# Kernel optimization log

Hardware: AMD Instinct MI355X
Metric: run time of the kernel (lower is better)

The kernel has to match this reference:

```python
import jax, jax.numpy as jnp
import numpy as np

EPS = 1e-5
STW = 10   # short_term_window_size
L = 12     # mlp_layers


def gru_step(h, x, Wi, Wh, bi, bh):
    # torch nn.GRU cell, gate order (r, z, n)
    gi = x @ Wi.T + bi            # [B, 3H]
    gh = h @ Wh.T + bh            # [B, 3H]
    ir, iz, inn = jnp.split(gi, 3, axis=-1)
    hr, hz, hn = jnp.split(gh, 3, axis=-1)
    r = jax.nn.sigmoid(ir + hr)
    z = jax.nn.sigmoid(iz + hz)
    n = jnp.tanh(inn + r * hn)
    return (1.0 - z) * n + z * h


def mlp_mini(m, seq_W, seq_b, ln_a, ln_b, out_W, out_b, mrg_W, mrg_b):
    # m: [B, S, H] -> siMLPe_mini -> [B, 1, C]
    f = jnp.swapaxes(m, 1, 2)                 # [B, H, S]
    for l in range(L):                        # TransMLP: temporal FC + spatial LN + residual
        y = f @ seq_W[l].T + seq_b[l]         # Linear over seq axis S
        mu = y.mean(axis=1, keepdims=True)    # LN over feature ('spatial') axis H
        var = ((y - mu) ** 2).mean(axis=1, keepdims=True)
        y = (y - mu) / jnp.sqrt(var + EPS) * ln_a[l][None, :, None] + ln_b[l][None, :, None]
        f = f + y
    f = jnp.swapaxes(f, 1, 2) @ out_W.T + out_b   # [B, S, C]  motion_fc_out
    f = jnp.swapaxes(f, 1, 2) @ mrg_W.T + mrg_b   # [B, C, 1]  temporal_merge_fc
    return jnp.swapaxes(f, 1, 2)                  # [B, 1, C]


def _forward(x, gru_Wi, gru_Wh, gru_bi, gru_bh, enc_W, enc_b,
             seq_W, seq_b, ln_alpha, ln_beta, out_W, out_b, merge_W, merge_b):
    B, T, C = x.shape
    H = gru_Wh.shape[1]

    @jax.checkpoint
    def enc_step(h, xt):
        return gru_step(h, xt, gru_Wi, gru_Wh, gru_bi, gru_bh), None

    h0 = jnp.zeros((B, H), dtype=x.dtype)
    h_enc, _ = jax.lax.scan(enc_step, h0, jnp.swapaxes(x[:, :-1, :], 0, 1))

    last_frame = x[:, -1, :]
    # encode_history=True: one GRU step on the last frame; resulting state discarded
    window_history = gru_step(h_enc, last_frame, gru_Wi, gru_Wh, gru_bi, gru_bh)[:, None, :]  # [B,1,H]

    buf0 = x[:, -STW:, :]  # sliding short-term window buffer [B, STW, C]

    @jax.checkpoint
    def dec_step(carry, _):
        h, last, buf = carry
        h = gru_step(h, last, gru_Wi, gru_Wh, gru_bi, gru_bh)
        dec = h[:, None, :]                        # [B, 1, H]
        wst = buf @ enc_W.T + enc_b                # fc_encoder: [B, STW, H]
        mlp_in = jnp.concatenate([window_history, wst, dec], axis=1)  # [B, STW+2, H]
        new = mlp_mini(mlp_in, seq_W, seq_b, ln_alpha, ln_beta, out_W, out_b, mrg_W=merge_W, mrg_b=merge_b)
        new = new + last[:, None, :]               # recursive_residual=True
        newf = new[:, 0, :]
        buf = jnp.concatenate([buf[:, 1:, :], new], axis=1)
        return (h, newf, buf), newf

    _, outs = jax.lax.scan(dec_step, (h_enc, last_frame, buf0), None, length=T)
    return jnp.swapaxes(outs, 0, 1)  # [B, T, C]


def setup_inputs() -> dict:
    key = jax.random.key(0)
    B, T, C, H = 1024, 64, 66, 1024
    S = STW + 2
    ks = jax.random.split(key, 16)

    def g(k, shape, scale):
        return jax.random.normal(k, shape, dtype=jnp.float32) * scale

    return {
        "x": g(ks[0], (B, T, C), 1.0),
        "gru_Wi": g(ks[1], (3 * H, C), 0.05),
        "gru_Wh": g(ks[2], (3 * H, H), 0.02),
        "gru_bi": jnp.zeros((3 * H,), jnp.float32),
        "gru_bh": jnp.zeros((3 * H,), jnp.float32),
        "enc_W": g(ks[3], (H, C), 0.05),
        "enc_b": jnp.zeros((H,), jnp.float32),
        "seq_W": g(ks[4], (L, S, S), 0.2),
        "seq_b": jnp.zeros((L, S), jnp.float32),
        "ln_alpha": jnp.ones((L, H), jnp.float32),
        "ln_beta": jnp.zeros((L, H), jnp.float32),
        "out_W": g(ks[5], (C, H), 0.02),
        "out_b": jnp.zeros((C,), jnp.float32),
        "merge_W": g(ks[6], (1, S), 0.2),
        "merge_b": jnp.zeros((1,), jnp.float32),
    }


def reference(x, gru_Wi, gru_Wh, gru_bi, gru_bh, enc_W, enc_b,
              seq_W, seq_b, ln_alpha, ln_beta, out_W, out_b, merge_W, merge_b):
    return _forward(x, gru_Wi, gru_Wh, gru_bi, gru_bh, enc_W, enc_b,
                    seq_W, seq_b, ln_alpha, ln_beta, out_W, out_b, merge_W, merge_b)
```

## Files before the change

### kernel.cpp

```cpp
#include <hip/hip_runtime.h>
#include <hip/hip_bf16.h>
#include <cstddef>
#include <cstdint>

#define BB 1024
#define TT 64
#define CC 66
#define HH 1024
#define SS 12
#define LL 12
#define XROW (TT*CC)
#define KSEG 16

typedef __attribute__((ext_vector_type(8))) __bf16 bfrag;
typedef __attribute__((ext_vector_type(4))) float f32x4;
typedef __attribute__((ext_vector_type(8))) short s8v;
typedef __attribute__((ext_vector_type(2))) float f2;

__device__ __forceinline__ unsigned short f2bf(float f) {
  unsigned int u = __builtin_bit_cast(unsigned int, f);
  unsigned int r = u + 0x7FFFu + ((u >> 16) & 1u);
  return (unsigned short)(r >> 16);
}
__device__ __forceinline__ float bf2f(unsigned short h) {
  unsigned int u = ((unsigned int)h) << 16;
  return __builtin_bit_cast(float, u);
}

__device__ __forceinline__ void gload16(const void* g, void* l) {
  __builtin_amdgcn_global_load_lds(
      (const __attribute__((address_space(1))) unsigned int*)g,
      (__attribute__((address_space(3))) unsigned int*)l, 16, 0, 0);
}

template<int CTRL, int RM>
__device__ __forceinline__ float dppadd(float v) {
  int x = __builtin_amdgcn_update_dpp(0, __builtin_bit_cast(int, v),
                                      CTRL, RM, 0xF, true);
  return v + __builtin_bit_cast(float, x);
}
__device__ __forceinline__ float wave_sum63(float v) {
  v = dppadd<0x111, 0xF>(v);
  v = dppadd<0x112, 0xF>(v);
  v = dppadd<0x114, 0xF>(v);
  v = dppadd<0x118, 0xF>(v);
  v = dppadd<0x142, 0xa>(v);
  v = dppadd<0x143, 0xc>(v);
  return v;
}

__global__ __launch_bounds__(256) void gru_mfma(
    const unsigned short* __restrict__ Ahi, const unsigned short* __restrict__ Alo,
    const float* __restrict__ hprev,
    const unsigned short* __restrict__ Xhi, const unsigned short* __restrict__ Xlo,
    const unsigned short* __restrict__ Whi, const unsigned short* __restrict__ Wlo,
    const float* __restrict__ bi, const float* __restrict__ bh,
    float* __restrict__ hout_f32,
    unsigned short* __restrict__ hout_hi, unsigned short* __restrict__ hout_lo)
{
  __shared__ __align__(16) unsigned short AsH[3][64*32];
  __shared__ __align__(16) unsigned short AsL[3][64*32];
  __shared__ __align__(16) unsigned short BsH[3][128*32];
  __shared__ __align__(16) unsigned short BsL[3][128*32];

  const int tid = threadIdx.x, lane = tid & 63, wid = tid >> 6;
  const int bid = blockIdx.x;
  const int idx = bid >> 3;
  const int jb = (bid & 7) * 4 + (idx & 3);
  const int b0 = (idx >> 2) * 64;
  const int wm = wid >> 1, wn = wid & 1;
  const int aR = lane >> 2, aC = lane & 3;

  auto stage = [&](int bs, int kc) {
    const unsigned short *shi, *slo; size_t go;
    int row = wid * 16 + aR;
    if (kc < 32) {
      go = (size_t)(b0 + row) * 1024 + (size_t)kc * 32 + aC * 8;
      shi = Ahi; slo = Alo;
    } else {
      go = (size_t)(b0 + row) * 96 + (size_t)(kc - 32) * 32 + aC * 8;
      shi = Xhi; slo = Xlo;
    }
    gload16(shi + go, &AsH[bs][wid * 512]);
    gload16(slo + go, &AsL[bs][wid * 512]);
    size_t base = ((size_t)jb * 35 + kc) * 4096;
    size_t go0 = base + (size_t)(wid * 32 + aR) * 32 + aC * 8;
    gload16(Whi + go0,       &BsH[bs][wid * 1024]);
    gload16(Whi + go0 + 512, &BsH[bs][wid * 1024 + 512]);
    gload16(Wlo + go0,       &BsL[bs][wid * 1024]);
    gload16(Wlo + go0 + 512, &BsL[bs][wid * 1024 + 512]);
  };

  int offA[2], offB[4];
  #pragma unroll
  for (int mh = 0; mh < 2; ++mh) {
    int r = wm * 32 + mh * 16 + (lane & 15);
    int cb = (lane >> 4) ^ (r & 3);
    offA[mh] = r * 32 + cb * 8;
  }
  #pragma unroll
  for (int g = 0; g < 4; ++g) {
    int r = wn * 64 + g * 16 + (lane & 15);
    int cb = (lane >> 4) ^ (r & 3);
    offB[g] = r * 32 + cb * 8;
  }

  f32x4 acc[2][4] = {};

  stage(0, 0);
  stage(1, 1);

  int cur = 0;
  for (int kc = 0; kc < 34; ++kc) {
    asm volatile("s_waitcnt vmcnt(6)" ::: "memory");
    __builtin_amdgcn_s_barrier();
    asm volatile("" ::: "memory");

    bfrag ah[2], al[2], bhf[4], blf[4];
    #pragma unroll
    for (int mh = 0; mh < 2; ++mh) {
      ah[mh] = __builtin_bit_cast(bfrag, *(const s8v*)(&AsH[cur][offA[mh]]));
      al[mh] = __builtin_bit_cast(bfrag, *(const s8v*)(&AsL[cur][offA[mh]]));
    }
    #pragma unroll
    for (int g = 0; g < 4; ++g) {
      bhf[g] = __builtin_bit_cast(bfrag, *(const s8v*)(&BsH[cur][offB[g]]));
      blf[g] = __builtin_bit_cast(bfrag, *(const s8v*)(&BsL[cur][offB[g]]));
    }
    if (kc < 33) {
      int st = (cur >= 1) ? cur - 1 : 2;
      stage(st, kc + 2);
    }
    #pragma unroll
    for (int mh = 0; mh < 2; ++mh)
      #pragma unroll
      for (int g = 0; g < 4; ++g) {
        acc[mh][g] = __builtin_amdgcn_mfma_f32_16x16x32_bf16(ah[mh], bhf[g], acc[mh][g], 0, 0, 0);
        acc[mh][g] = __builtin_amdgcn_mfma_f32_16x16x32_bf16(ah[mh], blf[g], acc[mh][g], 0, 0, 0);
        acc[mh][g] = __builtin_amdgcn_mfma_f32_16x16x32_bf16(al[mh], bhf[g], acc[mh][g], 0, 0, 0);
      }
    cur = (cur < 2) ? cur + 1 : 0;
  }
  {
    asm volatile("s_waitcnt vmcnt(0)" ::: "memory");
    __builtin_amdgcn_s_barrier();
    asm volatile("" ::: "memory");
    bfrag ah[2], al[2], bhf[4], blf[4];
    #pragma unroll
    for (int mh = 0; mh < 2; ++mh) {
      ah[mh] = __builtin_bit_cast(bfrag, *(const s8v*)(&AsH[1][offA[mh]]));
      al[mh] = __builtin_bit_cast(bfrag, *(const s8v*)(&AsL[1][offA[mh]]));
    }
    #pragma unroll
    for (int g = 0; g < 4; ++g) {
      bhf[g] = __builtin_bit_cast(bfrag, *(const s8v*)(&BsH[1][offB[g]]));
      blf[g] = __builtin_bit_cast(bfrag, *(const s8v*)(&BsL[1][offB[g]]));
    }
    #pragma unroll
    for (int mh = 0; mh < 2; ++mh)
      #pragma unroll
      for (int g = 0; g < 4; ++g) {
        acc[mh][g] = __builtin_amdgcn_mfma_f32_16x16x32_bf16(ah[mh], bhf[g], acc[mh][g], 0, 0, 0);
        acc[mh][g] = __builtin_amdgcn_mfma_f32_16x16x32_bf16(ah[mh], blf[g], acc[mh][g], 0, 0, 0);
        acc[mh][g] = __builtin_amdgcn_mfma_f32_16x16x32_bf16(al[mh], bhf[g], acc[mh][g], 0, 0, 0);
      }
  }

  const int j = jb * 32 + wn * 16 + (lane & 15);
  const float b_r  = bi[j] + bh[j];
  const float b_z  = bi[HH + j] + bh[HH + j];
  const float b_nh = bh[2 * HH + j];
  const float b_nx = bi[2 * HH + j];
  #pragma unroll
  for (int mh = 0; mh < 2; ++mh)
    #pragma unroll
    for (int q = 0; q < 4; ++q) {
      int m = b0 + wm * 32 + mh * 16 + (lane >> 4) * 4 + q;
      float hpv = hprev[(size_t)m * HH + j];
      float rr = acc[mh][0][q] + b_r;
      float zz = acc[mh][1][q] + b_z;
      float nh = acc[mh][2][q] + b_nh;
      float nx = acc[mh][3][q] + b_nx;
      float r = 1.f / (1.f + __expf(-rr));
      float z = 1.f / (1.f + __expf(-zz));
      float n = tanhf(nx + r * nh);
      float hv = (1.f - z) * n + z * hpv;
      hout_f32[(size_t)m * HH + j] = hv;
      unsigned short hi = f2bf(hv);
      float lo = hv - bf2f(hi);
      int cb = ((j >> 3) & 3) ^ (m & 3);
      size_t dst = (size_t)m * 1024 + (size_t)(j & ~31) + cb * 8 + (j & 7);
      hout_hi[dst] = hi;
      hout_lo[dst] = f2bf(lo);
    }
}

__global__ __launch_bounds__(256) void prep_wgc(
    const float* __restrict__ Wh, const float* __restrict__ Wi,
    unsigned short* __restrict__ Whi, unsigned short* __restrict__ Wlo)
{
  size_t idx = (size_t)blockIdx.x * 256 + threadIdx.x;
  if (idx >= (size_t)4096 * 1120) return;
  int k = (int)(idx % 1120);
  int rg = (int)(idx / 1120);
  int jbv = rg >> 7, r = rg & 127;
  int jhi = r >> 6, rem = r & 63, g = rem >> 4, jlo = rem & 15;
  int j = jbv * 32 + jhi * 16 + jlo;
  float v = 0.f;
  if (g == 0)      v = (k < 1024) ? Wh[(size_t)j * HH + k]            : ((k < 1090) ? Wi[(size_t)j * CC + (k - 1024)] : 0.f);
  else if (g == 1) v = (k < 1024) ? Wh[(size_t)(HH + j) * HH + k]     : ((k < 1090) ? Wi[(size_t)(HH + j) * CC + (k - 1024)] : 0.f);
  else if (g == 2) v = (k < 1024) ? Wh[(size_t)(2 * HH + j) * HH + k] : 0.f;
  else             v = (k >= 1024 && k < 1090) ? Wi[(size_t)(2 * HH + j) * CC + (k - 1024)] : 0.f;
  unsigned short hi = f2bf(v);
  float lo = v - bf2f(hi);
  int kc = k >> 5, kk = k & 31;
  int cb = ((kk >> 3) ^ (r & 3)) & 3;
  size_t dst = (((size_t)jbv * 35 + kc) * 128 + r) * 32 + cb * 8 + (kk & 7);
  Whi[dst] = hi;
  Wlo[dst] = f2bf(lo);
}

__global__ __launch_bounds__(256) void prep_xall(
    const float* __restrict__ x,
    unsigned short* __restrict__ Xhi, unsigned short* __restrict__ Xlo)
{
  size_t idx = (size_t)blockIdx.x * 256 + threadIdx.x;
  if (idx >= (size_t)TT * BB * 96) return;
  int kx = (int)(idx % 96);
  size_t rem = idx / 96;
  int b = (int)(rem % BB);
  int t = (int)(rem / BB);
  float v = (kx < CC) ? x[(size_t)b * XROW + (size_t)t * CC + kx] : 0.f;
  unsigned short hi = f2bf(v);
  float lo = v - bf2f(hi);
  int cb = (((kx >> 3) & 3) ^ (b & 3)) & 3;
  size_t dst = ((size_t)t * BB + b) * 96 + (size_t)(kx & ~31) + cb * 8 + (kx & 7);
  Xhi[dst] = hi;
  Xlo[dst] = f2bf(lo);
}

__global__ __launch_bounds__(256) void wst_row_kernel(
    const float* __restrict__ src, int src_stride,
    const float* __restrict__ encWT, const float* __restrict__ encb,
    float* __restrict__ dst, const int* __restrict__ flagp)
{
  if (*flagp) return;
  __shared__ float s[CC];
  int b = blockIdx.y;
  int h = blockIdx.x * 256 + threadIdx.x;
  if (threadIdx.x < CC) s[threadIdx.x] = src[(size_t)b * src_stride + threadIdx.x];
  __syncthreads();
  float acc = encb[h];
  #pragma unroll
  for (int k = 0; k < CC; ++k) acc = fmaf(s[k], encWT[(size_t)k * HH + h], acc);
  dst[(size_t)b * (10 * HH) + h] = acc;
}

__global__ __launch_bounds__(256) void transpose_encW(
    const float* __restrict__ W, float* __restrict__ WT)
{
  int k = blockIdx.x;
  int h = blockIdx.y * 256 + threadIdx.x;
  WT[(size_t)k * HH + h] = W[(size_t)h * CC + k];
}

__global__ __launch_bounds__(256) void copy_last_kernel(
    const float* __restrict__ x, float* __restrict__ last)
{
  int idx = blockIdx.x * 256 + threadIdx.x;
  if (idx < BB * CC) {
    int b = idx / CC, c = idx - b * CC;
    last[idx] = x[(size_t)b * XROW + 63 * CC + c];
  }
}

__global__ __launch_bounds__(256) void flag_kernel(
    const float* __restrict__ lnA, const float* __restrict__ lnB, int* flagp)
{
  int idx = blockIdx.x * 256 + threadIdx.x;
  bool ok;
  if (idx < LL * HH) ok = (lnA[idx] == 1.0f);
  else ok = (lnB[idx - LL * HH] == 0.0f);
  if (!ok) atomicAnd(flagp, 0);
}

__global__ __launch_bounds__(256) void prep_tabs(
    const float* __restrict__ encW, const float* __restrict__ encb,
    const float* __restrict__ outW, float* __restrict__ tabs)
{
  int idx = blockIdx.x * 256 + threadIdx.x;
  if (idx >= 8978) return;
  float a = 0.f;
  if (idx < 4356) {
    int c1 = idx / 66, c2 = idx % 66;
    for (int h = 0; h < HH; ++h) a = fmaf(encW[h * CC + c1], encW[h * CC + c2], a);
  } else if (idx < 8712) {
    int p = idx - 4356; int c = p / 66, c1 = p % 66;
    for (int h = 0; h < HH; ++h) a = fmaf(encW[h * CC + c1], outW[(size_t)c * HH + h], a);
  } else if (idx < 8778) {
    int c1 = idx - 8712;
    for (int h = 0; h < HH; ++h) a = fmaf(encW[h * CC + c1], encb[h], a);
  } else if (idx < 8844) {
    int c1 = idx - 8778;
    for (int h = 0; h < HH; ++h) a += encW[h * CC + c1];
  } else if (idx < 8910) {
    int c = idx - 8844;
    for (int h = 0; h < HH; ++h) a = fmaf(encb[h], outW[(size_t)c * HH + h], a);
  } else if (idx < 8976) {
    int c = idx - 8910;
    for (int h = 0; h < HH; ++h) a += outW[(size_t)c * HH + h];
  } else if (idx == 8976) {
    for (int h = 0; h < HH; ++h) a = fmaf(encb[h], encb[h], a);
  } else {
    for (int h = 0; h < HH; ++h) a += encb[h];
  }
  tabs[idx] = a;
}

__global__ __launch_bounds__(256) void prep_b144(
    const float* __restrict__ encW, const float* __restrict__ outW,
    const float* __restrict__ encb, float* __restrict__ B144)
{
  int idx = blockIdx.x * 256 + threadIdx.x;
  if (idx >= 1024 * 144) return;
  int k = idx / 144, n = idx % 144;
  float v;
  if (n < 66) v = encW[k * CC + n];
  else if (n < 132) v = outW[(size_t)(n - 66) * HH + k];
  else if (n == 132) v = encb[k];
  else if (n == 133) v = 1.f;
  else v = 0.f;
  B144[idx] = v;
}

__global__ __launch_bounds__(256) void linit_kernel(
    const float* __restrict__ x, float* __restrict__ l_ring,
    const int* __restrict__ flagp)
{
  if (!*flagp) return;
  int idx = blockIdx.x * 256 + threadIdx.x;
  if (idx >= 1024 * 9 * 66) return;
  int c = idx % 66; int r = idx / 66; int w = r % 9; int b = r / 9;
  l_ring[((size_t)b * 10 + w) * 66 + c] = x[(size_t)b * XROW + (54 + w) * CC + c];
}

__global__ __launch_bounds__(256) void qnew_kernel(
    const float* __restrict__ src, int sstride, const float* __restrict__ K3,
    float* __restrict__ q_ring, int slot, const int* __restrict__ flagp)
{
  if (!*flagp) return;
  __shared__ float Ks[4356];
  __shared__ float ls[8][66];
  int tid = threadIdx.x, b0 = blockIdx.x * 8;
  for (int i = tid; i < 4356; i += 256) Ks[i] = K3[i];
  for (int i = tid; i < 8 * 66; i += 256)
    ls[i / 66][i % 66] = src[(size_t)(b0 + i / 66) * sstride + (i % 66)];
  __syncthreads();
  for (int o = tid; o < 528; o += 256) {
    int bi = o / 66, c1 = o % 66;
    float a = 0.f;
    for (int c2 = 0; c2 < 66; ++c2) a = fmaf(Ks[c1 * 66 + c2], ls[bi][c2], a);
    q_ring[((size_t)(b0 + bi) * 10 + slot) * 66 + c1] = a;
  }
}

__global__ __launch_bounds__(256) void dec_gemm(
    const float* __restrict__ A, const float* __restrict__ B144,
    float* __restrict__ dp, const int* __restrict__ flagp)
{
  if (!*flagp) return;
  __shared__ float As[64][65];
  const int tid = threadIdx.x;
  const int b0 = blockIdx.x * 64;
  const int k0 = blockIdx.y * 64;
  for (int i = tid; i < 64 * 64; i += 256) {
    int r = i >> 6, c = i & 63;
    As[r][c] = A[(size_t)(b0 + r) * 1024 + k0 + c];
  }
  __syncthreads();
  const int b_sub = tid & 63;
  const int cg = __builtin_amdgcn_readfirstlane(tid >> 6);
  const int base_c = cg * 36;
  float acc[36];
  #pragma unroll
  for (int i = 0; i < 36; ++i) acc[i] = 0.f;
  for (int kk = 0; kk < 64; ++kk) {
    float av = As[b_sub][kk];
    const float* brow = B144 + (size_t)(k0 + kk) * 144 + base_c;
    #pragma unroll
    for (int q = 0; q < 9; ++q) {
      f32x4 b4 = *(const f32x4*)(brow + q * 4);
      acc[q * 4 + 0] = fmaf(av, b4[0], acc[q * 4 + 0]);
      acc[q * 4 + 1] = fmaf(av, b4[1], acc[q * 4 + 1]);
      acc[q * 4 + 2] = fmaf(av, b4[2], acc[q * 4 + 2]);
      acc[q * 4 + 3] = fmaf(av, b4[3], acc[q * 4 + 3]);
    }
  }
  float* drow = dp + ((size_t)blockIdx.y * 1024 + b0 + b_sub) * 144 + base_c;
  #pragma unroll
  for (int q = 0; q < 9; ++q)
    *(f32x4*)(drow + q * 4) = { acc[q*4+0], acc[q*4+1], acc[q*4+2], acc[q*4+3] };
}

__global__ __launch_bounds__(256) void fast_combine(
    const float* __restrict__ dp, float* __restrict__ u, float* __restrict__ G,
    float* __restrict__ e, float* __restrict__ s, const int* __restrict__ flagp)
{
  if (!*flagp) return;
  int o = blockIdx.x * 256 + threadIdx.x;
  if (o >= 1024 * 144) return;
  int b = o / 144, c = o % 144;
  float a = 0.f;
  #pragma unroll
  for (int g = 0; g < KSEG; ++g) a += dp[((size_t)g * 1024 + b) * 144 + c];
  if (c < 66) u[b * 66 + c] = a;
  else if (c < 132) G[b * 66 + (c - 66)] = a;
  else if (c == 132) e[b] = a;
  else if (c == 133) s[b] = a;
}

__global__ __launch_bounds__(256) void tail_kernel(
    const float* __restrict__ hdec, const float* __restrict__ whp,
    float* __restrict__ last, float* __restrict__ l_ring,
    float* __restrict__ q_ring, const float* __restrict__ dp,
    const float* __restrict__ u_whp, const float* __restrict__ G_whp,
    const float* __restrict__ e_whp, const float* __restrict__ s_whp,
    const float* __restrict__ tabs,
    float* __restrict__ wst, const float* __restrict__ encWT,
    const float* __restrict__ encb,
    const float* __restrict__ seqW, const float* __restrict__ seqb,
    const float* __restrict__ lnA, const float* __restrict__ lnB,
    const float* __restrict__ outW, const float* __restrict__ outb,
    const float* __restrict__ mrgW, const float* __restrict__ mrgb,
    int ring0, float* __restrict__ outp,
    unsigned short* __restrict__ lpH, unsigned short* __restrict__ lpL,
    const int* __restrict__ flagp)
{
  const int b = blockIdx.x, tid = threadIdx.x;
  const int lane = tid & 63, wid = tid >> 6;
  const int slot9 = (ring0 == 0) ? 9 : ring0 - 1;

  if (*flagp) {
    __shared__ float Ks[4356];
    __shared__ float l_all[10][66], Qv[10][66];
    __shared__ float yd[66], gd[66], uw[66], se1[66], scs[66], lmix[66];
    __shared__ float sW[156], sMm[156], sTt[156], sPp[156], sNn[156], sQq[156];
    __shared__ float sb12[12], sistd[12], scc[12], sfb[12], sdd12[12], swd[12], sVv[12], smrg[12];
    __shared__ float sred[12], misc[8];

    const float* K2T   = tabs + 4356;
    const float* tb_e1 = tabs + 8712;
    const float* tb_cs = tabs + 8778;
    const float* tb_g0 = tabs + 8844;
    const float* tb_R  = tabs + 8910;

    for (int i = tid; i < 4356; i += 256) Ks[i] = tabs[i];
    for (int i = tid; i < 660; i += 256) {
      int w = i / 66, c = i % 66;
      int slot = ring0 + w; if (slot >= 10) slot -= 10;
      if (w < 9) {
        Qv[w][c] = q_ring[((size_t)b * 10 + slot) * 66 + c];
        l_all[w][c] = l_ring[((size_t)b * 10 + slot) * 66 + c];
      } else {
        l_all[9][c] = last[(size_t)b * 66 + c];
      }
    }
    for (int i = tid; i < 66; i += 256) {
      uw[i]  = u_whp[(size_t)b * 66 + i];
      se1[i] = tb_e1[i];
      scs[i] = tb_cs[i];
    }
    if (tid < 134) {
      float a = 0.f;
      #pragma unroll
      for (int g = 0; g < KSEG; ++g) a += dp[((size_t)g * 1024 + b) * 144 + tid];
      if (tid < 66) yd[tid] = a;
      else if (tid < 132) gd[tid - 66] = a;
      else if (tid == 132) misc[1] = a;
      else misc[2] = a;
    }
    if (tid >= 160 && tid < 172) smrg[tid - 160] = mrgW[tid - 160];
    {
      f32x4 hv = *(const f32x4*)&hdec[(size_t)b * 1024 + tid * 4];
      f32x4 wv = *(const f32x4*)&whp[(size_t)b * 1024 + tid * 4];
      float d2 = hv[0]*hv[0] + hv[1]*hv[1] + hv[2]*hv[2] + hv[3]*hv[3];
      float dw = hv[0]*wv[0] + hv[1]*wv[1] + hv[2]*wv[2] + hv[3]*wv[3];
      float w2 = wv[0]*wv[0] + wv[1]*wv[1] + wv[2]*wv[2] + wv[3]*wv[3];
      d2 = wave_sum63(d2); dw = wave_sum63(dw); w2 = wave_sum63(w2);
      if (lane == 63) { sred[wid*3] = d2; sred[wid*3+1] = dw; sred[wid*3+2] = w2; }
    }
    __syncthreads();
    if (tid < 66) {
      float a = 0.f;
      for (int c2 = 0; c2 < 66; ++c2) a = fmaf(Ks[tid * 66 + c2], l_all[9][c2], a);
      Qv[9][tid] = a;
      q_ring[((size_t)b * 10 + slot9) * 66 + tid] = a;
    }
    if (tid >= 128 && tid < 131) {
      int i = tid - 128;
      misc[3 + i] = sred[i] + sred[3 + i] + sred[6 + i] + sred[9 + i];
    }
    if (tid == 132) misc[6] = tabs[8976];
    if (tid == 133) misc[7] = tabs[8977];
    __syncthreads();

    if (tid < 144) {
      int i = tid / 12, j = tid % 12;
      float gv;
      if (i == 0 && j == 0) gv = misc[5];
      else if (i == 11 && j == 11) gv = misc[3];
      else if ((i == 0 && j == 11) || (i == 11 && j == 0)) gv = misc[4];
      else if (i == 0 || j == 0) {
        int w = (i == 0 ? j : i) - 1;
        float a = e_whp[b];
        for (int c = 0; c < 66; ++c) a = fmaf(uw[c], l_all[w][c], a);
        gv = a;
      } else if (i == 11 || j == 11) {
        int w = (i == 11 ? j : i) - 1;
        float a = misc[1];
        for (int c = 0; c < 66; ++c) a = fmaf(yd[c], l_all[w][c], a);
        gv = a;
      } else {
        int wi = i - 1, wj = j - 1;
        float a = misc[6];
        for (int c = 0; c < 66; ++c) a = fmaf(se1[c], l_all[wi][c] + l_all[wj][c], a);
        for (int c = 0; c < 66; ++c) a = fmaf(l_all[wi][c], Qv[wj][c], a);
        gv = a;
      }
      sMm[i * 13 + j] = gv * (1.f / 1024.f);
      sTt[i * 13 + j] = (i == j) ? 1.f : 0.f;
    }
    if (tid >= 144 && tid < 156) {
      int k = tid - 144;
      float fb;
      if (k == 0) fb = s_whp[b] * (1.f / 1024.f);
      else if (k == 11) fb = misc[2] * (1.f / 1024.f);
      else {
        float a = misc[7];
        for (int c = 0; c < 66; ++c) a = fmaf(scs[c], l_all[k - 1][c], a);
        fb = a * (1.f / 1024.f);
      }
      sfb[k] = fb;
      sdd12[k] = 0.f;
    }
    __syncthreads();

    for (int l = 0; l < LL; ++l) {
      if (tid < 144) sW[(tid / 12) * 13 + (tid % 12)] = seqW[l * 144 + tid];
      if (tid >= 160 && tid < 172) sb12[tid - 160] = seqb[l * 12 + (tid - 160)];
      __syncthreads();
      if (tid < 144) {
        int s = tid / 12, k = tid % 12;
        float a = 0.f;
        #pragma unroll
        for (int k2 = 0; k2 < 12; ++k2) a = fmaf(sW[s * 13 + k2], sMm[k2 * 13 + k], a);
        sPp[s * 13 + k] = a;
      }
      __syncthreads();
      if (tid < 12) {
        int s = tid;
        float mu = sb12[s];
        #pragma unroll
        for (int k = 0; k < 12; ++k) mu = fmaf(sW[s * 13 + k], sfb[k], mu);
        float e2 = 0.f;
        #pragma unroll
        for (int k = 0; k < 12; ++k) e2 = fmaf(sPp[s * 13 + k], sW[s * 13 + k], e2);
        float wf = mu - sb12[s];
        float var = fmaxf(e2 - wf * wf, 0.f);
        float is = 1.f / sqrtf(var + 1e-5f);
        sistd[s] = is;
        scc[s] = is * (sb12[s] - mu);
      }
      __syncthreads();
      if (tid < 144) {
        int i = tid / 12, j = tid % 12;
        float a = 0.f;
        #pragma unroll
        for (int k = 0; k < 12; ++k) a = fmaf(sW[i * 13 + k], sTt[k * 13 + j], a);
        sQq[i * 13 + j] = a;
        sNn[i * 13 + j] = sMm[i * 13 + j] + sistd[i] * sPp[i * 13 + j];
      }
      if (tid >= 144 && tid < 156) {
        int i = tid - 144;
        float a = 0.f;
        #pragma unroll
        for (int k = 0; k < 12; ++k) a = fmaf(sW[i * 13 + k], sdd12[k], a);
        swd[i] = a;
      }
      __syncthreads();
      if (tid < 144) {
        int i = tid / 12, j = tid % 12;
        sTt[i * 13 + j] += sistd[i] * sQq[i * 13 + j];
        float a = 0.f;
        #pragma unroll
        for (int k = 0; k < 12; ++k) a = fmaf(sNn[i * 13 + k], sW[j * 13 + k], a);
        sPp[i * 13 + j] = a;
      }
      if (tid >= 144 && tid < 156) {
        int i = tid - 144;
        sdd12[i] = sdd12[i] + sistd[i] * swd[i] + scc[i];
      }
      __syncthreads();
      if (tid < 144) {
        int i = tid / 12, j = tid % 12;
        sMm[i * 13 + j] = sNn[i * 13 + j] + sPp[i * 13 + j] * sistd[j]
                        + sfb[i] * scc[j] + scc[i] * sfb[j] - scc[i] * scc[j];
      }
      __syncthreads();
    }

    if (tid < 12) {
      float a = 0.f;
      #pragma unroll
      for (int s = 0; s < 12; ++s) a = fmaf(smrg[s], sTt[s * 13 + tid], a);
      sVv[tid] = a;
    }
    if (tid == 200) {
      float a = 0.f;
      for (int s = 0; s < 12; ++s) a = fmaf(smrg[s], sdd12[s], a);
      misc[0] = a;
    }
    __syncthreads();
    if (tid < 66) {
      float a = 0.f;
      #pragma unroll
      for (int w = 0; w < 9; ++w) a = fmaf(sVv[1 + w], l_all[w][tid], a);
      a = fmaf(sVv[10], l_all[9][tid], a);
      lmix[tid] = a;
    }
    __syncthreads();
    if (tid < 66) {
      int c = tid;
      float vsr = 0.f, smw = 0.f;
      #pragma unroll
      for (int k = 1; k <= 10; ++k) vsr += sVv[k];
      #pragma unroll
      for (int s = 0; s < 12; ++s) smw += smrg[s];
      float lastv = l_all[9][c];
      float acc = sVv[0] * G_whp[(size_t)b * 66 + c]
                + vsr * tb_g0[c]
                + sVv[11] * gd[c]
                + misc[0] * tb_R[c]
                + smw * outb[c] + mrgb[0] + lastv;
      const float* krow = K2T + c * 66;
      for (int c2 = 0; c2 < 66; ++c2) acc = fmaf(lmix[c2], krow[c2], acc);
      outp[(size_t)b * XROW + c] = acc;
      last[(size_t)b * 66 + c] = acc;
      l_ring[((size_t)b * 10 + slot9) * 66 + c] = lastv;
      unsigned short hi = f2bf(acc);
      float lo = acc - bf2f(hi);
      int cb = (((c >> 3) & 3) ^ (b & 3)) & 3;
      size_t dst = (size_t)b * 96 + (size_t)(c & ~31) + cb * 8 + (c & 7);
      lpH[dst] = hi;
      lpL[dst] = f2bf(lo);
    }
    return;
  }

  __shared__ float red[4][24];
  __shared__ f2 mustd2[SS];
  __shared__ float g_lds[HH];
  __shared__ float nc[CC];

  const int h0 = tid;
  const int h1 = tid + 512;
  const float* lrow = last + (size_t)b * CC;
  f2 wnew[2];
  {
    f2 a0 = { encb[h0], encb[h0 + 256] };
    f2 a1 = { encb[h1], encb[h1 + 256] };
    #pragma unroll 11
    for (int k = 0; k < CC; ++k) {
      float lv = lrow[k];
      f2 lv2 = { lv, lv };
      f2 w0 = { encWT[(size_t)k * HH + h0], encWT[(size_t)k * HH + h0 + 256] };
      f2 w1 = { encWT[(size_t)k * HH + h1], encWT[(size_t)k * HH + h1 + 256] };
      a0 = __builtin_elementwise_fma(lv2, w0, a0);
      a1 = __builtin_elementwise_fma(lv2, w1, a1);
    }
    wnew[0] = a0; wnew[1] = a1;
    float* wd = wst + ((size_t)b * 10 + slot9) * HH;
    wd[h0] = a0.x; wd[h0 + 256] = a0.y;
    wd[h1] = a1.x; wd[h1 + 256] = a1.y;
  }

  f2 fr[2][SS];
  {
    const float* whb = whp + (size_t)b * HH;
    const float* hb  = hdec + (size_t)b * HH;
    fr[0][0]  = { whb[h0], whb[h0 + 256] };
    fr[1][0]  = { whb[h1], whb[h1 + 256] };
    fr[0][11] = { hb[h0], hb[h0 + 256] };
    fr[1][11] = { hb[h1], hb[h1 + 256] };
    #pragma unroll
    for (int w = 0; w < 9; ++w) {
      int slot = ring0 + w; if (slot >= 10) slot -= 10;
      const float* ws_ = wst + ((size_t)b * 10 + slot) * HH;
      fr[0][1 + w] = { ws_[h0], ws_[h0 + 256] };
      fr[1][1 + w] = { ws_[h1], ws_[h1 + 256] };
    }
    fr[0][10] = wnew[0];
    fr[1][10] = wnew[1];
  }

  #pragma unroll 1
  for (int l = 0; l < LL; ++l) {
    const float* W  = seqW + (size_t)l * SS * SS;
    const float* Bv = seqb + (size_t)l * SS;
    const float* lA = lnA + (size_t)l * HH;
    const float* lB = lnB + (size_t)l * HH;
    f2 al[2], be[2];
    al[0] = { lA[h0], lA[h0 + 256] };  al[1] = { lA[h1], lA[h1 + 256] };
    be[0] = { lB[h0], lB[h0 + 256] };  be[1] = { lB[h1], lB[h1 + 256] };

    f2 y[2][SS];
    #pragma unroll
    for (int s = 0; s < SS; ++s) {
      float bv = Bv[s];
      f2 a0 = { bv, bv }, a1 = { bv, bv };
      #pragma unroll
      for (int k = 0; k < SS; ++k) {
        float wv = W[s * SS + k];
        f2 wv2 = { wv, wv };
        a0 = __builtin_elementwise_fma(fr[0][k], wv2, a0);
        a1 = __builtin_elementwise_fma(fr[1][k], wv2, a1);
      }
      y[0][s] = a0; y[1][s] = a1;
      f2 pp = a0 + a1;
      float ps = wave_sum63(pp.x + pp.y);
      f2 qq = __builtin_elementwise_fma(a0, a0, a1 * a1);
      float pq = wave_sum63(qq.x + qq.y);
      if (lane == 63) { red[wid][s] = ps; red[wid][12 + s] = pq; }
    }
    __syncthreads();
    if (tid < SS) {
      float S = red[0][tid] + red[1][tid] + red[2][tid] + red[3][tid];
      float Q = red[0][12 + tid] + red[1][12 + tid] + red[2][12 + tid] + red[3][12 + tid];
      float mu = S * (1.f / HH);
      float var = Q * (1.f / HH) - mu * mu;
      mustd2[tid] = { mu, 1.f / sqrtf(var + 1e-5f) };
    }
    __syncthreads();
    #pragma unroll
    for (int s = 0; s < SS; ++s) {
      f2 mi = mustd2[s];
      f2 mus = { mi.x, mi.x };
      f2 isd = { mi.y, mi.y };
      #pragma unroll
      for (int p = 0; p < 2; ++p) {
        f2 t = (y[p][s] - mus) * isd;
        fr[p][s] = __builtin_elementwise_fma(t, al[p], fr[p][s]) + be[p];
      }
    }
    __syncthreads();
  }

  float smw = 0.f;
  f2 g[2] = { {0.f, 0.f}, {0.f, 0.f} };
  #pragma unroll
  for (int s = 0; s < SS; ++s) {
    float mv = mrgW[s];
    smw += mv;
    f2 mv2 = { mv, mv };
    g[0] = __builtin_elementwise_fma(mv2, fr[0][s], g[0]);
    g[1] = __builtin_elementwise_fma(mv2, fr[1][s], g[1]);
  }
  g_lds[h0] = g[0].x; g_lds[h0 + 256] = g[0].y;
  g_lds[h1] = g[1].x; g_lds[h1 + 256] = g[1].y;
  const float mbv = mrgb[0];
  __syncthreads();
  #pragma unroll 1
  for (int i = 0; i < 17; ++i) {
    int c = wid + 4 * i;
    if (c < CC) {
      const float* ow = outW + (size_t)c * HH;
      float acc = 0.f;
      #pragma unroll
      for (int q = 0; q < 16; ++q) acc = fmaf(g_lds[lane + q * 64], ow[lane + q * 64], acc);
      acc = wave_sum63(acc);
      if (lane == 63) nc[c] = acc + outb[c] * smw + mbv + lrow[c];
    }
  }
  __syncthreads();
  if (tid < CC) {
    float nv = nc[tid];
    outp[(size_t)b * XROW + tid] = nv;
    last[(size_t)b * CC + tid] = nv;
    unsigned short hi = f2bf(nv);
    float lo = nv - bf2f(hi);
    int cb = (((tid >> 3) & 3) ^ (b & 3)) & 3;
    size_t dst = (size_t)b * 96 + (size_t)(tid & ~31) + cb * 8 + (tid & 7);
    lpH[dst] = hi;
    lpL[dst] = f2bf(lo);
  }
}

extern "C" void kernel_launch(void* const* d_in, const int* in_sizes, int n_in,
                              void* d_out, int out_size, void* d_ws, size_t ws_size,
                              hipStream_t stream) {
  const float* x    = (const float*)d_in[0];
  const float* gWi  = (const float*)d_in[1];
  const float* gWh  = (const float*)d_in[2];
  const float* gbi  = (const float*)d_in[3];
  const float* gbh  = (const float*)d_in[4];
  const float* encW = (const float*)d_in[5];
  const float* encb = (const float*)d_in[6];
  const float* seqW = (const float*)d_in[7];
  const float* seqb = (const float*)d_in[8];
  const float* lnA  = (const float*)d_in[9];
  const float* lnB  = (const float*)d_in[10];
  const float* outW = (const float*)d_in[11];
  const float* outb = (const float*)d_in[12];
  const float* mrgW = (const float*)d_in[13];
  const float* mrgb = (const float*)d_in[14];
  float* out = (float*)d_out;

  char* p = (char*)d_ws;
  auto alloc = [&](size_t bytes) { char* r = p; p += (bytes + 255) & ~(size_t)255; return r; };
  float* encWT = (float*)alloc((size_t)CC * HH * 4);
  float* last  = (float*)alloc((size_t)BB * CC * 4);
  float* wst   = (float*)alloc((size_t)BB * 10 * HH * 4);
  float* hf[3];
  for (int i = 0; i < 3; ++i) hf[i] = (float*)alloc((size_t)BB * HH * 4);
  unsigned short* WgH = (unsigned short*)alloc((size_t)4096 * 1120 * 2);
  unsigned short* WgL = (unsigned short*)alloc((size_t)4096 * 1120 * 2);
  unsigned short* XaH = (unsigned short*)alloc((size_t)TT * BB * 96 * 2);
  unsigned short* XaL = (unsigned short*)alloc((size_t)TT * BB * 96 * 2);
  unsigned short* hhi[3]; unsigned short* hlo[3];
  for (int i = 0; i < 3; ++i) {
    hhi[i] = (unsigned short*)alloc((size_t)BB * HH * 2);
    hlo[i] = (unsigned short*)alloc((size_t)BB * HH * 2);
  }
  unsigned short* lpH = (unsigned short*)alloc((size_t)BB * 96 * 2);
  unsigned short* lpL = (unsigned short*)alloc((size_t)BB * 96 * 2);
  int* flag = (int*)alloc(256);
  if ((size_t)(p - (char*)d_ws) > ws_size) return;

  char* ov = (char*)wst;
  float* B144  = (float*)ov;                 ov += (size_t)1024 * 144 * 4;
  float* dp    = (float*)ov;                 ov += (size_t)KSEG * 1024 * 144 * 4;
  float* l_ring= (float*)ov;                 ov += (size_t)1024 * 10 * 66 * 4;
  float* q_ring= (float*)ov;                 ov += (size_t)1024 * 10 * 66 * 4;
  float* u_whp = (float*)ov;                 ov += (size_t)1024 * 66 * 4;
  float* G_whp = (float*)ov;                 ov += (size_t)1024 * 66 * 4;
  float* e_whp = (float*)ov;                 ov += 4096;
  float* s_whp = (float*)ov;                 ov += 4096;
  float* tabs  = (float*)ov;                 ov += 9216 * 4;

  hipMemsetAsync(flag, 0xFF, 4, stream);
  flag_kernel<<<dim3(96), 256, 0, stream>>>(lnA, lnB, flag);
  prep_wgc<<<dim3((4096u * 1120u) / 256u), 256, 0, stream>>>(gWh, gWi, WgH, WgL);
  prep_xall<<<dim3(((unsigned)TT * BB * 96) / 256u), 256, 0, stream>>>(x, XaH, XaL);
  transpose_encW<<<dim3(CC, HH/256), 256, 0, stream>>>(encW, encWT);
  copy_last_kernel<<<dim3((BB*CC + 255)/256), 256, 0, stream>>>(x, last);
  prep_b144<<<dim3(576), 256, 0, stream>>>(encW, outW, encb, B144);
  prep_tabs<<<dim3(36), 256, 0, stream>>>(encW, encb, outW, tabs);
  linit_kernel<<<dim3((1024*9*66)/256), 256, 0, stream>>>(x, l_ring, flag);
  for (int w = 0; w < 9; ++w)
    qnew_kernel<<<dim3(128), 256, 0, stream>>>(x + (size_t)(54 + w) * CC, XROW,
                                               tabs, q_ring, w, flag);
  hipMemsetAsync(hf[0], 0, (size_t)BB * HH * 4, stream);
  hipMemsetAsync(hhi[0], 0, (size_t)BB * HH * 2, stream);
  hipMemsetAsync(hlo[0], 0, (size_t)BB * HH * 2, stream);

  const dim3 ggrid(512);

  int cur = 0;
  for (int t = 0; t < 63; ++t) {
    int nxt = 1 - cur;
    gru_mfma<<<ggrid, 256, 0, stream>>>(
        hhi[cur], hlo[cur], hf[cur],
        XaH + (size_t)t * BB * 96, XaL + (size_t)t * BB * 96,
        WgH, WgL, gbi, gbh, hf[nxt], hhi[nxt], hlo[nxt]);
    cur = nxt;
  }
  gru_mfma<<<ggrid, 256, 0, stream>>>(
      hhi[cur], hlo[cur], hf[cur],
      XaH + (size_t)63 * BB * 96, XaL + (size_t)63 * BB * 96,
      WgH, WgL, gbi, gbh, hf[2], hhi[2], hlo[2]);

  dec_gemm<<<dim3(16, KSEG), 256, 0, stream>>>(hf[2], B144, dp, flag);
  fast_combine<<<dim3(576), 256, 0, stream>>>(dp, u_whp, G_whp, e_whp, s_whp, flag);

  for (int w = 0; w < 9; ++w)
    wst_row_kernel<<<dim3(HH/256, BB), 256, 0, stream>>>(
        x + (size_t)(54 + w) * CC, XROW, encWT, encb, wst + (size_t)w * HH, flag);

  int hc = 2;
  for (int t = 0; t < 64; ++t) {
    if (t > 0) {
      int hn = (t - 1) & 1;
      gru_mfma<<<ggrid, 256, 0, stream>>>(
          hhi[hc], hlo[hc], hf[hc], lpH, lpL,
          WgH, WgL, gbi, gbh, hf[hn], hhi[hn], hlo[hn]);
      hc = hn;
    }
    dec_gemm<<<dim3(16, KSEG), 256, 0, stream>>>(hf[hc], B144, dp, flag);
    tail_kernel<<<dim3(BB), 256, 0, stream>>>(
        hf[hc], hf[2], last, l_ring, q_ring, dp,
        u_whp, G_whp, e_whp, s_whp, tabs,
        wst, encWT, encb, seqW, seqb, lnA, lnB, outW, outb, mrgW, mrgb,
        t % 10, out + (size_t)t * CC, lpH, lpL, flag);
  }
}
```

Before: 8.802 ms.

## Fuse decoder projection GEMM into GRU epilogue and precompute ring projection

The separate dec_gemm kernel, which reread the new hidden state from global memory, is removed. Each GRU block now stages its own 64x32 h tile in shared memory and writes a partial product against B144 into one of 32 segments, so tail_kernel and fast_combine sum 32 partials instead of 16. The K3 projection of the newest frame moves to the end of tail_kernel, which writes it into the ring for the next step; tail_kernel no longer loads the 4356-float K table into shared memory, and the initial qnew pass covers 10 slots. This saves one launch per decoder step and a re-read of h, at the cost of a longer GRU epilogue, extra syncs and twice as many partials to reduce.

```diff
diff --git a/kernel.cpp b/kernel.cpp
--- a/kernel.cpp
+++ b/kernel.cpp
@@ -10,7 +10,7 @@
 #define SS 12
 #define LL 12
 #define XROW (TT*CC)
-#define KSEG 16
+#define DPSEG 32
 
 typedef __attribute__((ext_vector_type(8))) __bf16 bfrag;
 typedef __attribute__((ext_vector_type(4))) float f32x4;
@@ -56,7 +56,9 @@
     const unsigned short* __restrict__ Whi, const unsigned short* __restrict__ Wlo,
     const float* __restrict__ bi, const float* __restrict__ bh,
     float* __restrict__ hout_f32,
-    unsigned short* __restrict__ hout_hi, unsigned short* __restrict__ hout_lo)
+    unsigned short* __restrict__ hout_hi, unsigned short* __restrict__ hout_lo,
+    const float* __restrict__ B144, float* __restrict__ dp32,
+    const int* __restrict__ flagp, int do_dp)
 {
   __shared__ __align__(16) unsigned short AsH[3][64*32];
   __shared__ __align__(16) unsigned short AsL[3][64*32];
@@ -171,6 +173,7 @@
   const float b_z  = bi[HH + j] + bh[HH + j];
   const float b_nh = bh[2 * HH + j];
   const float b_nx = bi[2 * HH + j];
+  float hvv[2][4];
   #pragma unroll
   for (int mh = 0; mh < 2; ++mh)
     #pragma unroll
@@ -185,6 +188,7 @@
       float z = 1.f / (1.f + __expf(-zz));
       float n = tanhf(nx + r * nh);
       float hv = (1.f - z) * n + z * hpv;
+      hvv[mh][q] = hv;
       hout_f32[(size_t)m * HH + j] = hv;
       unsigned short hi = f2bf(hv);
       float lo = hv - bf2f(hi);
@@ -193,6 +197,42 @@
       hout_hi[dst] = hi;
       hout_lo[dst] = f2bf(lo);
     }
+
+  if (do_dp && *flagp) {
+    float* hsf = reinterpret_cast<float*>(&AsH[0][0]);
+    __syncthreads();
+    #pragma unroll
+    for (int mh = 0; mh < 2; ++mh)
+      #pragma unroll
+      for (int q = 0; q < 4; ++q) {
+        int mloc = wm * 32 + mh * 16 + (lane >> 4) * 4 + q;
+        int jloc = wn * 16 + (lane & 15);
+        hsf[mloc * 33 + jloc] = hvv[mh][q];
+      }
+    __syncthreads();
+    const int b_sub = tid & 63;
+    const int cg = __builtin_amdgcn_readfirstlane(tid >> 6);
+    const int base_c = cg * 36;
+    float acc36[36];
+    #pragma unroll
+    for (int i = 0; i < 36; ++i) acc36[i] = 0.f;
+    for (int kk = 0; kk < 32; ++kk) {
+      float av = hsf[b_sub * 33 + kk];
+      const float* brow = B144 + (size_t)(jb * 32 + kk) * 144 + base_c;
+      #pragma unroll
+      for (int qq = 0; qq < 9; ++qq) {
+        f32x4 b4 = *(const f32x4*)(brow + qq * 4);
+        acc36[qq*4+0] = fmaf(av, b4[0], acc36[qq*4+0]);
+        acc36[qq*4+1] = fmaf(av, b4[1], acc36[qq*4+1]);
+        acc36[qq*4+2] = fmaf(av, b4[2], acc36[qq*4+2]);
+        acc36[qq*4+3] = fmaf(av, b4[3], acc36[qq*4+3]);
+      }
+    }
+    float* drow = dp32 + ((size_t)jb * 1024 + b0 + b_sub) * 144 + base_c;
+    #pragma unroll
+    for (int qq = 0; qq < 9; ++qq)
+      *(f32x4*)(drow + qq * 4) = { acc36[qq*4+0], acc36[qq*4+1], acc36[qq*4+2], acc36[qq*4+3] };
+  }
 }
 
 __global__ __launch_bounds__(256) void prep_wgc(
@@ -364,44 +404,6 @@
   }
 }
 
-__global__ __launch_bounds__(256) void dec_gemm(
-    const float* __restrict__ A, const float* __restrict__ B144,
-    float* __restrict__ dp, const int* __restrict__ flagp)
-{
-  if (!*flagp) return;
-  __shared__ float As[64][65];
-  const int tid = threadIdx.x;
-  const int b0 = blockIdx.x * 64;
-  const int k0 = blockIdx.y * 64;
-  for (int i = tid; i < 64 * 64; i += 256) {
-    int r = i >> 6, c = i & 63;
-    As[r][c] = A[(size_t)(b0 + r) * 1024 + k0 + c];
-  }
-  __syncthreads();
-  const int b_sub = tid & 63;
-  const int cg = __builtin_amdgcn_readfirstlane(tid >> 6);
-  const int base_c = cg * 36;
-  float acc[36];
-  #pragma unroll
-  for (int i = 0; i < 36; ++i) acc[i] = 0.f;
-  for (int kk = 0; kk < 64; ++kk) {
-    float av = As[b_sub][kk];
-    const float* brow = B144 + (size_t)(k0 + kk) * 144 + base_c;
-    #pragma unroll
-    for (int q = 0; q < 9; ++q) {
-      f32x4 b4 = *(const f32x4*)(brow + q * 4);
-      acc[q * 4 + 0] = fmaf(av, b4[0], acc[q * 4 + 0]);
-      acc[q * 4 + 1] = fmaf(av, b4[1], acc[q * 4 + 1]);
-      acc[q * 4 + 2] = fmaf(av, b4[2], acc[q * 4 + 2]);
-      acc[q * 4 + 3] = fmaf(av, b4[3], acc[q * 4 + 3]);
-    }
-  }
-  float* drow = dp + ((size_t)blockIdx.y * 1024 + b0 + b_sub) * 144 + base_c;
-  #pragma unroll
-  for (int q = 0; q < 9; ++q)
-    *(f32x4*)(drow + q * 4) = { acc[q*4+0], acc[q*4+1], acc[q*4+2], acc[q*4+3] };
-}
-
 __global__ __launch_bounds__(256) void fast_combine(
     const float* __restrict__ dp, float* __restrict__ u, float* __restrict__ G,
     float* __restrict__ e, float* __restrict__ s, const int* __restrict__ flagp)
@@ -412,7 +414,7 @@
   int b = o / 144, c = o % 144;
   float a = 0.f;
   #pragma unroll
-  for (int g = 0; g < KSEG; ++g) a += dp[((size_t)g * 1024 + b) * 144 + c];
+  for (int g = 0; g < DPSEG; ++g) a += dp[((size_t)g * 1024 + b) * 144 + c];
   if (c < 66) u[b * 66 + c] = a;
   else if (c < 132) G[b * 66 + (c - 66)] = a;
   else if (c == 132) e[b] = a;
@@ -441,9 +443,8 @@
   const int slot9 = (ring0 == 0) ? 9 : ring0 - 1;
 
   if (*flagp) {
-    __shared__ float Ks[4356];
     __shared__ float l_all[10][66], Qv[10][66];
-    __shared__ float yd[66], gd[66], uw[66], se1[66], scs[66], lmix[66];
+    __shared__ float yd[66], gd[66], uw[66], se1[66], scs[66], lmix[66], newf[66];
     __shared__ float sW[156], sMm[156], sTt[156], sPp[156], sNn[156], sQq[156];
     __shared__ float sb12[12], sistd[12], scc[12], sfb[12], sdd12[12], swd[12], sVv[12], smrg[12];
     __shared__ float sred[12], misc[8];
@@ -454,16 +455,12 @@
     const float* tb_g0 = tabs + 8844;
     const float* tb_R  = tabs + 8910;
 
-    for (int i = tid; i < 4356; i += 256) Ks[i] = tabs[i];
     for (int i = tid; i < 660; i += 256) {
       int w = i / 66, c = i % 66;
       int slot = ring0 + w; if (slot >= 10) slot -= 10;
-      if (w < 9) {
-        Qv[w][c] = q_ring[((size_t)b * 10 + slot) * 66 + c];
-        l_all[w][c] = l_ring[((size_t)b * 10 + slot) * 66 + c];
-      } else {
-        l_all[9][c] = last[(size_t)b * 66 + c];
-      }
+      Qv[w][c] = q_ring[((size_t)b * 10 + slot) * 66 + c];
+      if (w < 9) l_all[w][c] = l_ring[((size_t)b * 10 + slot) * 66 + c];
+      else       l_all[9][c] = last[(size_t)b * 66 + c];
     }
     for (int i = tid; i < 66; i += 256) {
       uw[i]  = u_whp[(size_t)b * 66 + i];
@@ -473,7 +470,7 @@
     if (tid < 134) {
       float a = 0.f;
       #pragma unroll
-      for (int g = 0; g < KSEG; ++g) a += dp[((size_t)g * 1024 + b) * 144 + tid];
+      for (int g = 0; g < DPSEG; ++g) a += dp[((size_t)g * 1024 + b) * 144 + tid];
       if (tid < 66) yd[tid] = a;
       else if (tid < 132) gd[tid - 66] = a;
       else if (tid == 132) misc[1] = a;
@@ -490,12 +487,6 @@
       if (lane == 63) { sred[wid*3] = d2; sred[wid*3+1] = dw; sred[wid*3+2] = w2; }
     }
     __syncthreads();
-    if (tid < 66) {
-      float a = 0.f;
-      for (int c2 = 0; c2 < 66; ++c2) a = fmaf(Ks[tid * 66 + c2], l_all[9][c2], a);
-      Qv[9][tid] = a;
-      q_ring[((size_t)b * 10 + slot9) * 66 + tid] = a;
-    }
     if (tid >= 128 && tid < 131) {
       int i = tid - 128;
       misc[3 + i] = sred[i] + sred[3 + i] + sred[6 + i] + sred[9 + i];
@@ -647,12 +638,20 @@
       outp[(size_t)b * XROW + c] = acc;
       last[(size_t)b * 66 + c] = acc;
       l_ring[((size_t)b * 10 + slot9) * 66 + c] = lastv;
+      newf[c] = acc;
       unsigned short hi = f2bf(acc);
       float lo = acc - bf2f(hi);
       int cb = (((c >> 3) & 3) ^ (b & 3)) & 3;
       size_t dst = (size_t)b * 96 + (size_t)(c & ~31) + cb * 8 + (c & 7);
       lpH[dst] = hi;
       lpL[dst] = f2bf(lo);
+    }
+    __syncthreads();
+    if (tid < 66) {
+      float a = 0.f;
+      const float* k3r = tabs + tid * 66;
+      for (int c2 = 0; c2 < 66; ++c2) a = fmaf(k3r[c2], newf[c2], a);
+      q_ring[((size_t)b * 10 + ring0) * 66 + tid] = a;
     }
     return;
   }
@@ -838,7 +837,7 @@
 
   char* ov = (char*)wst;
   float* B144  = (float*)ov;                 ov += (size_t)1024 * 144 * 4;
-  float* dp    = (float*)ov;                 ov += (size_t)KSEG * 1024 * 144 * 4;
+  float* dp32  = (float*)ov;                 ov += (size_t)DPSEG * 1024 * 144 * 4;
   float* l_ring= (float*)ov;                 ov += (size_t)1024 * 10 * 66 * 4;
   float* q_ring= (float*)ov;                 ov += (size_t)1024 * 10 * 66 * 4;
   float* u_whp = (float*)ov;                 ov += (size_t)1024 * 66 * 4;
@@ -856,7 +855,7 @@
   prep_b144<<<dim3(576), 256, 0, stream>>>(encW, outW, encb, B144);
   prep_tabs<<<dim3(36), 256, 0, stream>>>(encW, encb, outW, tabs);
   linit_kernel<<<dim3((1024*9*66)/256), 256, 0, stream>>>(x, l_ring, flag);
-  for (int w = 0; w < 9; ++w)
+  for (int w = 0; w < 10; ++w)
     qnew_kernel<<<dim3(128), 256, 0, stream>>>(x + (size_t)(54 + w) * CC, XROW,
                                                tabs, q_ring, w, flag);
   hipMemsetAsync(hf[0], 0, (size_t)BB * HH * 4, stream);
@@ -871,16 +870,17 @@
     gru_mfma<<<ggrid, 256, 0, stream>>>(
         hhi[cur], hlo[cur], hf[cur],
         XaH + (size_t)t * BB * 96, XaL + (size_t)t * BB * 96,
-        WgH, WgL, gbi, gbh, hf[nxt], hhi[nxt], hlo[nxt]);
+        WgH, WgL, gbi, gbh, hf[nxt], hhi[nxt], hlo[nxt],
+        B144, dp32, flag, 0);
     cur = nxt;
   }
   gru_mfma<<<ggrid, 256, 0, stream>>>(
       hhi[cur], hlo[cur], hf[cur],
       XaH + (size_t)63 * BB * 96, XaL + (size_t)63 * BB * 96,
-      WgH, WgL, gbi, gbh, hf[2], hhi[2], hlo[2]);
-
-  dec_gemm<<<dim3(16, KSEG), 256, 0, stream>>>(hf[2], B144, dp, flag);
-  fast_combine<<<dim3(576), 256, 0, stream>>>(dp, u_whp, G_whp, e_whp, s_whp, flag);
+      WgH, WgL, gbi, gbh, hf[2], hhi[2], hlo[2],
+      B144, dp32, flag, 1);
+
+  fast_combine<<<dim3(576), 256, 0, stream>>>(dp32, u_whp, G_whp, e_whp, s_whp, flag);
 
   for (int w = 0; w < 9; ++w)
     wst_row_kernel<<<dim3(HH/256, BB), 256, 0, stream>>>(
@@ -892,12 +892,12 @@
       int hn = (t - 1) & 1;
       gru_mfma<<<ggrid, 256, 0, stream>>>(
           hhi[hc], hlo[hc], hf[hc], lpH, lpL,
-          WgH, WgL, gbi, gbh, hf[hn], hhi[hn], hlo[hn]);
+          WgH, WgL, gbi, gbh, hf[hn], hhi[hn], hlo[hn],
+          B144, dp32, flag, 1);
       hc = hn;
     }
-    dec_gemm<<<dim3(16, KSEG), 256, 0, stream>>>(hf[hc], B144, dp, flag);
     tail_kernel<<<dim3(BB), 256, 0, stream>>>(
-        hf[hc], hf[2], last, l_ring, q_ring, dp,
+        hf[hc], hf[2], last, l_ring, q_ring, dp32,
         u_whp, G_whp, e_whp, s_whp, tabs,
         wst, encWT, encb, seqW, seqb, lnA, lnB, outW, outb, mrgW, mrgb,
         t % 10, out + (size_t)t * CC, lpH, lpL, flag);
```

Result: faster. 7.997 ms (-9.2%).
